# Kernel optimization log

Hardware: AMD Instinct MI355X
Metric: run time of the kernel (lower is better)

Reference implementation:

```python
import jax, jax.numpy as jnp
import numpy as np

DIM = 1024
HEADS = 16

def setup_inputs() -> dict:
    key = jax.random.key(0)
    k1, k2, k3, k4 = jax.random.split(key, 4)
    x = jax.random.normal(k1, (2, 2048, DIM), dtype=jnp.float32)
    # torch Linear weights are [out_features, in_features]
    w_qkv = jax.random.normal(k2, (3 * DIM, DIM), dtype=jnp.float32) * (DIM ** -0.5)
    w_out = jax.random.normal(k3, (DIM, DIM), dtype=jnp.float32) * (DIM ** -0.5)
    b_out = jax.random.normal(k4, (DIM,), dtype=jnp.float32) * 0.01
    return {"x": x, "w_qkv": w_qkv, "w_out": w_out, "b_out": b_out}

def reference(x, w_qkv, w_out, b_out):
    b, n, dim = x.shape
    h = HEADS
    d = dim // h
    scale = dim ** -0.5  # NOTE: full dim, faithful to source
    qkv = x @ w_qkv.T                       # [b, n, 3*dim]
    qkv = qkv.reshape(b, n, 3, h, d)        # split (qkv h d)
    q, k, v = (qkv[:, :, i].transpose(0, 2, 1, 3) for i in range(3))  # [b, h, n, d]
    scores = jnp.einsum('bhid,bhjd->bhij', q, k) * scale
    weights = jax.nn.softmax(scores, axis=-1)
    out = jnp.einsum('bhij,bhjd->bhid', weights, v)  # [b, h, n, d]
    out = out.transpose(0, 2, 1, 3).reshape(b, n, dim)
    return out @ w_out.T + b_out
```

## Files before the change

### kernel.cpp

```cpp
#include <hip/hip_runtime.h>

#define DIM   1024
#define HEADS 16
#define NSEQ  2048
#define BATCH 2

typedef unsigned short u16;
typedef unsigned long long u64;
typedef __attribute__((ext_vector_type(8))) short bf16x8;
typedef __attribute__((ext_vector_type(4))) float f32x4;
typedef __attribute__((ext_vector_type(16))) float f32x16;

__device__ __forceinline__ u16 f2b(float f) {
  union { float f; unsigned u; } v; v.f = f;
  unsigned r = (v.u + 0x7fffu + ((v.u >> 16) & 1u)) >> 16;
  return (u16)r;
}

__device__ __forceinline__ void g2l16(const u16* g, u16* l) {
  __builtin_amdgcn_global_load_lds(
      (const __attribute__((address_space(1))) void*)g,
      (__attribute__((address_space(3))) void*)l, 16, 0, 0);
}

#define N4_X  (4096 * 1024 / 4)
#define N4_W  (3072 * 1024 / 4)
#define N4_O  (1024 * 1024 / 4)
__global__ void cvt_all(const float* __restrict__ x, const float* __restrict__ wqkv,
                        const float* __restrict__ wout,
                        u16* __restrict__ xb, u16* __restrict__ wqkvb,
                        u16* __restrict__ woutb, float s) {
  int i = blockIdx.x * blockDim.x + threadIdx.x;
  const float* src; u16* dst; int j; float m = 1.0f;
  if (i < N4_X)            { src = x;    dst = xb;    j = i; }
  else if (i < N4_X + N4_W){ src = wqkv; dst = wqkvb; j = i - N4_X; if (j < 1024 * 1024 / 4) m = s; }
  else                     { src = wout; dst = woutb; j = i - N4_X - N4_W; }
  float4 f = ((const float4*)src)[j];
  union { u16 s[4]; u64 ll; } o;
  o.s[0] = f2b(f.x * m); o.s[1] = f2b(f.y * m);
  o.s[2] = f2b(f.z * m); o.s[3] = f2b(f.w * m);
  ((u64*)dst)[j] = o.ll;
}

__global__ __launch_bounds__(256, 2)
void gemm_bt(const u16* __restrict__ A, const u16* __restrict__ Bt,
             void* __restrict__ C, const float* __restrict__ bias,
             int M, int Nc, int K, int bf16_out) {
  __shared__ u16 As[128 * 128];
  __shared__ u16 Bs[128 * 128];
  const int tid  = threadIdx.x;
  const int wave = tid >> 6, lane = tid & 63;
  const int l15  = lane & 15, quad = lane >> 4;
  const int m0 = blockIdx.y * 128, n0 = blockIdx.x * 128;
  const int wm = (wave >> 1) * 64, wn = (wave & 1) * 64;
  const int rb = wave * 32;

  f32x4 acc[4][4] = {};

  for (int kt = 0; kt < K; kt += 128) {
#pragma unroll
    for (int c = 0; c < 8; ++c) {
      int r  = rb + c * 4 + (lane >> 4);
      int ck = (lane & 15) ^ (r & 15);
      g2l16(A  + (size_t)(m0 + r) * K + kt + ck * 8, &As[(rb + c * 4) * 128]);
      g2l16(Bt + (size_t)(n0 + r) * K + kt + ck * 8, &Bs[(rb + c * 4) * 128]);
    }
    __syncthreads();
#pragma unroll
    for (int ks = 0; ks < 4; ++ks) {
      bf16x8 a[4], b[4];
      int ch = ks * 4 + quad;
#pragma unroll
      for (int i = 0; i < 4; ++i) {
        int ra  = wm + i * 16 + l15;
        a[i] = *(const bf16x8*)&As[ra * 128 + ((ch ^ (ra & 15)) << 3)];
        int rb2 = wn + i * 16 + l15;
        b[i] = *(const bf16x8*)&Bs[rb2 * 128 + ((ch ^ (rb2 & 15)) << 3)];
      }
#pragma unroll
      for (int i = 0; i < 4; ++i)
#pragma unroll
        for (int j = 0; j < 4; ++j)
          acc[i][j] = __builtin_amdgcn_mfma_f32_16x16x32_bf16(a[i], b[j], acc[i][j], 0, 0, 0);
    }
    __syncthreads();
  }

#pragma unroll
  for (int i = 0; i < 4; ++i)
#pragma unroll
    for (int j = 0; j < 4; ++j) {
      int row = m0 + wm + i * 16 + quad * 4;
      int col = n0 + wn + j * 16 + l15;
#pragma unroll
      for (int r = 0; r < 4; ++r) {
        float v = acc[i][j][r];
        if (bf16_out) ((u16*)C)[(size_t)(row + r) * Nc + col] = f2b(v);
        else          ((float*)C)[(size_t)(row + r) * Nc + col] = v + bias[col];
      }
    }
}

__global__ __launch_bounds__(256, 2)
void gemm_bt_n64(const u16* __restrict__ A, const u16* __restrict__ Bt,
                 float* __restrict__ C, const float* __restrict__ bias,
                 int M, int Nc, int K) {
  __shared__ u16 As[128 * 128];
  __shared__ u16 Bs[64 * 128];
  const int tid  = threadIdx.x;
  const int wave = tid >> 6, lane = tid & 63;
  const int l15  = lane & 15, quad = lane >> 4;
  const int m0 = blockIdx.y * 128, n0 = blockIdx.x * 64;
  const int wm = wave * 32;

  f32x4 acc[2][4] = {};

  for (int kt = 0; kt < K; kt += 128) {
#pragma unroll
    for (int c = 0; c < 8; ++c) {
      int r  = wave * 32 + c * 4 + (lane >> 4);
      int ck = (lane & 15) ^ (r & 15);
      g2l16(A + (size_t)(m0 + r) * K + kt + ck * 8, &As[(wave * 32 + c * 4) * 128]);
    }
#pragma unroll
    for (int c = 0; c < 4; ++c) {
      int r  = wave * 16 + c * 4 + (lane >> 4);
      int ck = (lane & 15) ^ (r & 15);
      g2l16(Bt + (size_t)(n0 + r) * K + kt + ck * 8, &Bs[(wave * 16 + c * 4) * 128]);
    }
    __syncthreads();
#pragma unroll
    for (int ks = 0; ks < 4; ++ks) {
      bf16x8 a[2], b[4];
      int ch = ks * 4 + quad;
#pragma unroll
      for (int i = 0; i < 2; ++i) {
        int ra = wm + i * 16 + l15;
        a[i] = *(const bf16x8*)&As[ra * 128 + ((ch ^ (ra & 15)) << 3)];
      }
#pragma unroll
      for (int j = 0; j < 4; ++j) {
        int rb2 = j * 16 + l15;
        b[j] = *(const bf16x8*)&Bs[rb2 * 128 + ((ch ^ (rb2 & 15)) << 3)];
      }
#pragma unroll
      for (int i = 0; i < 2; ++i)
#pragma unroll
        for (int j = 0; j < 4; ++j)
          acc[i][j] = __builtin_amdgcn_mfma_f32_16x16x32_bf16(a[i], b[j], acc[i][j], 0, 0, 0);
    }
    __syncthreads();
  }

#pragma unroll
  for (int i = 0; i < 2; ++i)
#pragma unroll
    for (int j = 0; j < 4; ++j) {
      int row = m0 + wm + i * 16 + quad * 4;
      int col = n0 + j * 16 + l15;
#pragma unroll
      for (int r = 0; r < 4; ++r)
        C[(size_t)(row + r) * Nc + col] = acc[i][j][r] + bias[col];
    }
}

__global__ __launch_bounds__(256, 2)
void attn(const u16* __restrict__ qkv, u16* __restrict__ outp) {
  __shared__ u16 Ks[2][128 * 64];
  __shared__ u16 Vts[2][64 * 128];
  const int tid  = threadIdx.x;
  const int wave = tid >> 6, lane = tid & 63;
  const int l31  = lane & 31, h = lane >> 5;
  const int b = blockIdx.x >> 4, hd = blockIdx.x & 15;
  const int q0 = blockIdx.y * 128;
  const u16* base = qkv + (size_t)b * NSEQ * 3072;
  const int qoff = hd * 64, koff = DIM + hd * 64, voff = 2 * DIM + hd * 64;
  const int dc = tid & 7, j0l = (tid >> 3) * 4;
  const int vchunk = (j0l >> 4) * 2 + ((j0l >> 2) & 1);
  const int vboff  = 4 * ((j0l >> 3) & 1);

  union V4 { uint4 q; u16 s[8]; };
  union PA { unsigned w[4]; bf16x8 f; };

#pragma unroll
  for (int c = 0; c < 4; ++c) {
    int bse = wave * 32 + c * 8;
    g2l16(base + (size_t)(q0 + bse + (lane >> 3)) * 3072 + qoff + (((lane & 7) ^ ((lane >> 3) & 7)) << 3),
          &Ks[0][bse * 64]);
  }
  __syncthreads();
  bf16x8 qf[4];
  {
    int qr = wave * 32 + l31;
#pragma unroll
    for (int kd = 0; kd < 4; ++kd)
      qf[kd] = *(const bf16x8*)&Ks[0][qr * 64 + (((kd * 2 + h) ^ (qr & 7)) << 3)];
  }
  __syncthreads();

  V4 vr[4];
#pragma unroll
  for (int c = 0; c < 4; ++c) {
    int bse = wave * 32 + c * 8;
    g2l16(base + (size_t)(bse + (lane >> 3)) * 3072 + koff + (((lane & 7) ^ ((lane >> 3) & 7)) << 3),
          &Ks[0][bse * 64]);
  }
#pragma unroll
  for (int e = 0; e < 4; ++e)
    vr[e].q = *(const uint4*)(base + (size_t)(j0l + e) * 3072 + voff + dc * 8);
#pragma unroll
  for (int u = 0; u < 8; ++u) {
    int d = dc * 8 + u;
    unsigned w0 = (unsigned)vr[0].s[u] | ((unsigned)vr[1].s[u] << 16);
    unsigned w1 = (unsigned)vr[2].s[u] | ((unsigned)vr[3].s[u] << 16);
    *(u64*)&Vts[0][d * 128 + ((vchunk ^ ((d + (d >> 3)) & 15)) << 3) + vboff] =
        (u64)w0 | ((u64)w1 << 32);
  }
  __syncthreads();

  float lrun = 0.0f;
  f32x16 oacc[2] = {};

  for (int t = 0; t < 16; ++t) {
    const int pbuf = t & 1;
    if (t < 15) {
      const int j0n = (t + 1) * 128;
#pragma unroll
      for (int c = 0; c < 4; ++c) {
        int bse = wave * 32 + c * 8;
        g2l16(base + (size_t)(j0n + bse + (lane >> 3)) * 3072 + koff + (((lane & 7) ^ ((lane >> 3) & 7)) << 3),
              &Ks[pbuf ^ 1][bse * 64]);
      }
#pragma unroll
      for (int e = 0; e < 4; ++e)
        vr[e].q = *(const uint4*)(base + (size_t)(j0n + j0l + e) * 3072 + voff + dc * 8);
    }

    f32x16 sc[4] = {};
    __builtin_amdgcn_s_setprio(1);
#pragma unroll
    for (int kd = 0; kd < 4; ++kd) {
      bf16x8 kb[4];
#pragma unroll
      for (int ni = 0; ni < 4; ++ni) {
        int kr = ni * 32 + l31;
        kb[ni] = *(const bf16x8*)&Ks[pbuf][kr * 64 + (((kd * 2 + h) ^ (kr & 7)) << 3)];
      }
#pragma unroll
      for (int ni = 0; ni < 4; ++ni)
        sc[ni] = __builtin_amdgcn_mfma_f32_32x32x16_bf16(kb[ni], qf[kd], sc[ni], 0, 0, 0);
    }
    __builtin_amdgcn_s_setprio(0);

    PA pa[8];
#pragma unroll
    for (int ni = 0; ni < 4; ++ni) {
      f32x16 p;
#pragma unroll
      for (int r = 0; r < 16; ++r) p[r] = __builtin_amdgcn_exp2f(sc[ni][r]);
      float s0 = (p[0] + p[1]) + (p[2] + p[3]);
      float s1 = (p[4] + p[5]) + (p[6] + p[7]);
      float s2 = (p[8] + p[9]) + (p[10] + p[11]);
      float s3 = (p[12] + p[13]) + (p[14] + p[15]);
      lrun += (s0 + s1) + (s2 + s3);
#pragma unroll
      for (int ks2 = 0; ks2 < 2; ++ks2)
#pragma unroll
        for (int i = 0; i < 4; ++i) {
          unsigned lo = __float_as_uint(p[8 * ks2 + 2 * i])     + 0x8000u;
          unsigned hi = __float_as_uint(p[8 * ks2 + 2 * i + 1]) + 0x8000u;
          pa[2 * ni + ks2].w[i] = __builtin_amdgcn_perm(hi, lo, 0x07060302u);
        }
    }

    __builtin_amdgcn_s_setprio(1);
#pragma unroll
    for (int f = 0; f < 8; ++f) {
      bf16x8 vb[2];
#pragma unroll
      for (int nd = 0; nd < 2; ++nd) {
        int d = nd * 32 + l31;
        vb[nd] = *(const bf16x8*)&Vts[pbuf][d * 128 + (((2 * f + h) ^ ((d + (d >> 3)) & 15)) << 3)];
      }
#pragma unroll
      for (int nd = 0; nd < 2; ++nd)
        oacc[nd] = __builtin_amdgcn_mfma_f32_32x32x16_bf16(pa[f].f, vb[nd], oacc[nd], 0, 0, 0);
    }
    __builtin_amdgcn_s_setprio(0);

    if (t < 15) {
#pragma unroll
      for (int u = 0; u < 8; ++u) {
        int d = dc * 8 + u;
        unsigned w0 = (unsigned)vr[0].s[u] | ((unsigned)vr[1].s[u] << 16);
        unsigned w1 = (unsigned)vr[2].s[u] | ((unsigned)vr[3].s[u] << 16);
        *(u64*)&Vts[pbuf ^ 1][d * 128 + ((vchunk ^ ((d + (d >> 3)) & 15)) << 3) + vboff] =
            (u64)w0 | ((u64)w1 << 32);
      }
    }
    __syncthreads();
  }

  float l = lrun + __shfl_xor(lrun, 32, 64);
  float linv = 1.0f / l;
#pragma unroll
  for (int r = 0; r < 16; ++r) {
    int rowloc = (r & 3) + 8 * (r >> 2) + 4 * h;
    float lb = __shfl(linv, rowloc, 64);
    int row = q0 + wave * 32 + rowloc;
#pragma unroll
    for (int nd = 0; nd < 2; ++nd)
      outp[((size_t)b * NSEQ + row) * DIM + hd * 64 + nd * 32 + l31] = f2b(oacc[nd][r] * lb);
  }
}

extern "C" void kernel_launch(void* const* d_in, const int* in_sizes, int n_in,
                              void* d_out, int out_size, void* d_ws, size_t ws_size,
                              hipStream_t stream) {
  const float* x     = (const float*)d_in[0];
  const float* w_qkv = (const float*)d_in[1];
  const float* w_out = (const float*)d_in[2];
  const float* b_out = (const float*)d_in[3];
  float* outp = (float*)d_out;

  u16* xb    = (u16*)d_ws;
  u16* wqkvb = xb    + (size_t)4096 * 1024;
  u16* woutb = wqkvb + (size_t)3072 * 1024;
  u16* qkvb  = woutb + (size_t)1024 * 1024;
  u16* attnb = qkvb  + (size_t)4096 * 3072;

  const float C2 = 0.03125f * 1.44269504088896340736f;

  cvt_all<<<(N4_X + N4_W + N4_O) / 256, 256, 0, stream>>>(x, w_qkv, w_out,
                                                          xb, wqkvb, woutb, C2);

  gemm_bt<<<dim3(24, 32), 256, 0, stream>>>(xb, wqkvb, qkvb, nullptr, 4096, 3072, 1024, 1);
  attn<<<dim3(32, 16), 256, 0, stream>>>(qkvb, attnb);
  gemm_bt_n64<<<dim3(16, 32), 256, 0, stream>>>(attnb, woutb, outp, b_out, 4096, 1024, 1024);
}
```

Measured before the change: 177.5 us.

## Double-buffer GEMM LDS tiles with K-step 64 and prefetch next tile

Both projection GEMM kernels switch from a single 128-wide K tile to two 64-wide LDS buffers. The next K tile is loaded asynchronously with global_load_lds while MFMAs run on the current buffer, which leaves one barrier per iteration instead of two. The XOR swizzle changes from 16 to 8 chunks to match the narrower tile. The aim is to hide global-load latency behind compute. The cost is twice as many loop iterations, and correctness relies on the barrier waiting for the outstanding LDS-direct loads.

```diff
diff --git a/kernel.cpp b/kernel.cpp
--- a/kernel.cpp
+++ b/kernel.cpp
@@ -46,36 +46,52 @@
 void gemm_bt(const u16* __restrict__ A, const u16* __restrict__ Bt,
              void* __restrict__ C, const float* __restrict__ bias,
              int M, int Nc, int K, int bf16_out) {
-  __shared__ u16 As[128 * 128];
-  __shared__ u16 Bs[128 * 128];
+  __shared__ u16 As[2][128 * 64];
+  __shared__ u16 Bs[2][128 * 64];
   const int tid  = threadIdx.x;
   const int wave = tid >> 6, lane = tid & 63;
   const int l15  = lane & 15, quad = lane >> 4;
   const int m0 = blockIdx.y * 128, n0 = blockIdx.x * 128;
   const int wm = (wave >> 1) * 64, wn = (wave & 1) * 64;
   const int rb = wave * 32;
+  const int rowoff = lane >> 3, ckx = lane & 7;
 
   f32x4 acc[4][4] = {};
-
-  for (int kt = 0; kt < K; kt += 128) {
-#pragma unroll
-    for (int c = 0; c < 8; ++c) {
-      int r  = rb + c * 4 + (lane >> 4);
-      int ck = (lane & 15) ^ (r & 15);
-      g2l16(A  + (size_t)(m0 + r) * K + kt + ck * 8, &As[(rb + c * 4) * 128]);
-      g2l16(Bt + (size_t)(n0 + r) * K + kt + ck * 8, &Bs[(rb + c * 4) * 128]);
-    }
+  const int nk = K >> 6;
+
+#pragma unroll
+  for (int c = 0; c < 4; ++c) {
+    int bse = rb + c * 8;
+    int r  = bse + rowoff;
+    int ck = ckx ^ (r & 7);
+    g2l16(A  + (size_t)(m0 + r) * K + ck * 8, &As[0][bse * 64]);
+    g2l16(Bt + (size_t)(n0 + r) * K + ck * 8, &Bs[0][bse * 64]);
+  }
+
+  for (int t = 0; t < nk; ++t) {
+    const int buf = t & 1;
     __syncthreads();
-#pragma unroll
-    for (int ks = 0; ks < 4; ++ks) {
+    if (t + 1 < nk) {
+      const int kt = (t + 1) << 6;
+#pragma unroll
+      for (int c = 0; c < 4; ++c) {
+        int bse = rb + c * 8;
+        int r  = bse + rowoff;
+        int ck = ckx ^ (r & 7);
+        g2l16(A  + (size_t)(m0 + r) * K + kt + ck * 8, &As[buf ^ 1][bse * 64]);
+        g2l16(Bt + (size_t)(n0 + r) * K + kt + ck * 8, &Bs[buf ^ 1][bse * 64]);
+      }
+    }
+#pragma unroll
+    for (int ks = 0; ks < 2; ++ks) {
       bf16x8 a[4], b[4];
       int ch = ks * 4 + quad;
 #pragma unroll
       for (int i = 0; i < 4; ++i) {
         int ra  = wm + i * 16 + l15;
-        a[i] = *(const bf16x8*)&As[ra * 128 + ((ch ^ (ra & 15)) << 3)];
+        a[i] = *(const bf16x8*)&As[buf][ra * 64 + ((ch ^ (ra & 7)) << 3)];
         int rb2 = wn + i * 16 + l15;
-        b[i] = *(const bf16x8*)&Bs[rb2 * 128 + ((ch ^ (rb2 & 15)) << 3)];
+        b[i] = *(const bf16x8*)&Bs[buf][rb2 * 64 + ((ch ^ (rb2 & 7)) << 3)];
       }
 #pragma unroll
       for (int i = 0; i < 4; ++i)
@@ -83,7 +99,6 @@
         for (int j = 0; j < 4; ++j)
           acc[i][j] = __builtin_amdgcn_mfma_f32_16x16x32_bf16(a[i], b[j], acc[i][j], 0, 0, 0);
     }
-    __syncthreads();
   }
 
 #pragma unroll
@@ -105,43 +120,66 @@
 void gemm_bt_n64(const u16* __restrict__ A, const u16* __restrict__ Bt,
                  float* __restrict__ C, const float* __restrict__ bias,
                  int M, int Nc, int K) {
-  __shared__ u16 As[128 * 128];
-  __shared__ u16 Bs[64 * 128];
+  __shared__ u16 As[2][128 * 64];
+  __shared__ u16 Bs[2][64 * 64];
   const int tid  = threadIdx.x;
   const int wave = tid >> 6, lane = tid & 63;
   const int l15  = lane & 15, quad = lane >> 4;
   const int m0 = blockIdx.y * 128, n0 = blockIdx.x * 64;
   const int wm = wave * 32;
+  const int rowoff = lane >> 3, ckx = lane & 7;
 
   f32x4 acc[2][4] = {};
-
-  for (int kt = 0; kt < K; kt += 128) {
-#pragma unroll
-    for (int c = 0; c < 8; ++c) {
-      int r  = wave * 32 + c * 4 + (lane >> 4);
-      int ck = (lane & 15) ^ (r & 15);
-      g2l16(A + (size_t)(m0 + r) * K + kt + ck * 8, &As[(wave * 32 + c * 4) * 128]);
-    }
-#pragma unroll
-    for (int c = 0; c < 4; ++c) {
-      int r  = wave * 16 + c * 4 + (lane >> 4);
-      int ck = (lane & 15) ^ (r & 15);
-      g2l16(Bt + (size_t)(n0 + r) * K + kt + ck * 8, &Bs[(wave * 16 + c * 4) * 128]);
-    }
+  const int nk = K >> 6;
+
+#pragma unroll
+  for (int c = 0; c < 4; ++c) {
+    int bse = wave * 32 + c * 8;
+    int r  = bse + rowoff;
+    int ck = ckx ^ (r & 7);
+    g2l16(A + (size_t)(m0 + r) * K + ck * 8, &As[0][bse * 64]);
+  }
+#pragma unroll
+  for (int c = 0; c < 2; ++c) {
+    int bse = wave * 16 + c * 8;
+    int r  = bse + rowoff;
+    int ck = ckx ^ (r & 7);
+    g2l16(Bt + (size_t)(n0 + r) * K + ck * 8, &Bs[0][bse * 64]);
+  }
+
+  for (int t = 0; t < nk; ++t) {
+    const int buf = t & 1;
     __syncthreads();
-#pragma unroll
-    for (int ks = 0; ks < 4; ++ks) {
+    if (t + 1 < nk) {
+      const int kt = (t + 1) << 6;
+#pragma unroll
+      for (int c = 0; c < 4; ++c) {
+        int bse = wave * 32 + c * 8;
+        int r  = bse + rowoff;
+        int ck = ckx ^ (r & 7);
+        g2l16(A + (size_t)(m0 + r) * K + kt + ck * 8, &As[buf ^ 1][bse * 64]);
+      }
+#pragma unroll
+      for (int c = 0; c < 2; ++c) {
+        int bse = wave * 16 + c * 8;
+        int r  = bse + rowoff;
+        int ck = ckx ^ (r & 7);
+        g2l16(Bt + (size_t)(n0 + r) * K + kt + ck * 8, &Bs[buf ^ 1][bse * 64]);
+      }
+    }
+#pragma unroll
+    for (int ks = 0; ks < 2; ++ks) {
       bf16x8 a[2], b[4];
       int ch = ks * 4 + quad;
 #pragma unroll
       for (int i = 0; i < 2; ++i) {
         int ra = wm + i * 16 + l15;
-        a[i] = *(const bf16x8*)&As[ra * 128 + ((ch ^ (ra & 15)) << 3)];
+        a[i] = *(const bf16x8*)&As[buf][ra * 64 + ((ch ^ (ra & 7)) << 3)];
       }
 #pragma unroll
       for (int j = 0; j < 4; ++j) {
         int rb2 = j * 16 + l15;
-        b[j] = *(const bf16x8*)&Bs[rb2 * 128 + ((ch ^ (rb2 & 15)) << 3)];
+        b[j] = *(const bf16x8*)&Bs[buf][rb2 * 64 + ((ch ^ (rb2 & 7)) << 3)];
       }
 #pragma unroll
       for (int i = 0; i < 2; ++i)
@@ -149,7 +187,6 @@
         for (int j = 0; j < 4; ++j)
           acc[i][j] = __builtin_amdgcn_mfma_f32_16x16x32_bf16(a[i], b[j], acc[i][j], 0, 0, 0);
     }
-    __syncthreads();
   }
 
 #pragma unroll
```

Result: slower. 184.8 us (+4.1%).
